# Kernel tuning notes

Measured on AMD Instinct MI355X. Metric: run time of the kernel, lower is better.

The kernel has to match this reference:

```python
import jax, jax.numpy as jnp
import numpy as np

RANK, A1, A2, B1, B2, BATCH = 16, 64, 8, 64, 8, 32768

def setup_inputs() -> dict:
    key = jax.random.key(0)
    kx, ks, ka, kb, kbias = jax.random.split(key, 5)
    # Params drawn as small gaussians (stand-in for xavier init; exact init
    x = jax.random.normal(kx, (BATCH, A1 * B1), dtype=jnp.float32)
    s = jax.random.normal(ks, (A1, A2), dtype=jnp.float32)
    a = jax.random.normal(ka, (RANK, A1, A2), dtype=jnp.float32) * 0.05
    b = jax.random.normal(kb, (RANK, B1, B2), dtype=jnp.float32) * 0.05
    bias = jax.random.normal(kbias, (A2 * B2,), dtype=jnp.float32)
    return {"x": x, "s": s, "a": a, "b": b, "bias": bias}

def reference(x, s, a, b, bias):
    # sa[r] = s * a[r]   (elementwise scale shared across ranks)
    sa = s[None, :, :] * a                                    # (r, a1, a2)
    # w = sum_r kron(sa[r], b[r]): w[i*b1+k, j*b2+l] = sum_r sa[r,i,j] b[r,k,l]
    # w is only (a1*b1, a2*b2) = (4096, 64), cheap to materialize here.
    w = jnp.einsum('rij,rkl->ikjl', sa, b).reshape(A1 * B1, A2 * B2)
    return x @ w + bias[None, :]                              # (batch, a2*b2)
```

## Files before the change

kernel.cpp:

```cpp
#include <hip/hip_runtime.h>
#include <hip/hip_bf16.h>

#define RANK 16
#define BATCH 32768
#define K_DIM 4096
#define N_DIM 64
#define CHUNK 128
#define NCHUNK 32
#define ROWB 64

typedef __bf16 bf16x8 __attribute__((ext_vector_type(8)));
typedef float floatx4 __attribute__((ext_vector_type(4)));
typedef unsigned short ushort8 __attribute__((ext_vector_type(8)));

__device__ inline unsigned short f2bf(float f) {
  unsigned u = __builtin_bit_cast(unsigned, f);
  u += 0x7fffu + ((u >> 16) & 1u);
  return (unsigned short)(u >> 16);
}

__device__ inline bf16x8 cvt8(float4 a0, float4 a1) {
  ushort8 au;
  au[0] = f2bf(a0.x); au[1] = f2bf(a0.y); au[2] = f2bf(a0.z); au[3] = f2bf(a0.w);
  au[4] = f2bf(a1.x); au[5] = f2bf(a1.y); au[6] = f2bf(a1.z); au[7] = f2bf(a1.w);
  return __builtin_bit_cast(bf16x8, au);
}

__global__ __launch_bounds__(256) void build_wT(
    const float* __restrict__ s, const float* __restrict__ a,
    const float* __restrict__ b, unsigned short* __restrict__ wT) {
  int idx = blockIdx.x * 256 + threadIdx.x;
  int n = idx >> 12;
  int k = idx & 4095;
  int j = n >> 3, l = n & 7;
  int i = k >> 6, kk = k & 63;
  float acc = 0.f;
  #pragma unroll
  for (int r = 0; r < RANK; ++r) {
    acc += a[r * 512 + i * 8 + j] * b[r * 512 + kk * 8 + l];
  }
  acc *= s[i * 8 + j];
  wT[idx] = f2bf(acc);
}

__global__ __launch_bounds__(256, 2) void kron_gemm(
    const float* __restrict__ x, const unsigned short* __restrict__ wT,
    const float* __restrict__ bias, float* __restrict__ out) {
  __shared__ __align__(16) float As[2][ROWB * CHUNK];

  const int tid   = threadIdx.x;
  const int lane  = tid & 63;
  const int wave  = tid >> 6;
  const int ln15  = lane & 15;
  const int kseg  = lane >> 4;
  const int u     = lane & 31;
  const int rhalf = lane >> 5;
  const int m0    = blockIdx.x * ROWB;
  const int sw    = (ln15 & 7) << 4;

  const unsigned short* wp = wT + (size_t)(wave * 16 + ln15) * K_DIM + kseg * 8;

  floatx4 acc[4] = {};

  auto stage = [&](int buf, int c) {
    #pragma unroll
    for (int j = 0; j < 8; ++j) {
      const int row = wave * 16 + 2 * j + rhalf;
      const int sb  = (u * 16) ^ ((row & 7) << 4);
      const float* src = x + (size_t)(m0 + row) * K_DIM + c * CHUNK + (sb >> 2);
      float* dst = &As[buf][(wave * 16 + 2 * j) * CHUNK];
      __builtin_amdgcn_global_load_lds(
          (const __attribute__((address_space(1))) void*)(const void*)src,
          (__attribute__((address_space(3))) void*)(void*)dst,
          16, 0, 0);
    }
  };

  stage(0, 0);
  __syncthreads();

  for (int c = 0; c < NCHUNK; ++c) {
    const int cur = c & 1;
    if (c + 1 < NCHUNK) stage(cur ^ 1, c + 1);

    const char* Ab = (const char*)&As[cur][0];
    #pragma unroll
    for (int t = 0; t < 4; ++t) {
      bf16x8 wf = *(const bf16x8*)(wp + c * CHUNK + t * 32);
      #pragma unroll
      for (int f = 0; f < 4; ++f) {
        const int row = 16 * f + ln15;
        const int b0  = t * 128 + kseg * 32;
        float4 lo = *(const float4*)(Ab + row * 512 + ((b0)      ^ sw));
        float4 hi = *(const float4*)(Ab + row * 512 + ((b0 + 16) ^ sw));
        acc[f] = __builtin_amdgcn_mfma_f32_16x16x32_bf16(cvt8(lo, hi), wf, acc[f], 0, 0, 0);
      }
    }
    __syncthreads();
  }

  const int col = wave * 16 + ln15;
  const float bv = bias[col];
  #pragma unroll
  for (int f = 0; f < 4; ++f) {
    float* op = out + (size_t)(m0 + 16 * f + kseg * 4) * N_DIM + col;
    #pragma unroll
    for (int r = 0; r < 4; ++r)
      op[(size_t)r * N_DIM] = acc[f][r] + bv;
  }
}

extern "C" void kernel_launch(void* const* d_in, const int* in_sizes, int n_in,
                              void* d_out, int out_size, void* d_ws, size_t ws_size,
                              hipStream_t stream) {
  const float* x    = (const float*)d_in[0];
  const float* s    = (const float*)d_in[1];
  const float* a    = (const float*)d_in[2];
  const float* b    = (const float*)d_in[3];
  const float* bias = (const float*)d_in[4];
  float* out = (float*)d_out;
  unsigned short* wT = (unsigned short*)d_ws;

  build_wT<<<(N_DIM * K_DIM) / 256, 256, 0, stream>>>(s, a, b, wT);
  kron_gemm<<<BATCH / ROWB, 256, 0, stream>>>(x, wT, bias, out);
}
```

Baseline: 138.3 us.

## Triple-buffer x and W tiles in LDS with 32x32 MFMA tiling

Each k-step now stages both the x tile and a fragment-ordered bf16 W tile into LDS through async global_load_lds into a three-deep ring. Waits use explicit vmcnt counts and raw barriers, replacing the previous double buffer, which read W straight from global memory per wave. The weight build kernel now writes W pre-permuted into the MFMA fragment layout. Compute switches from four 16x16x32 MFMAs per wave to one 32x32x16 MFMA per k-subtile on a 2x2 wave grid, with a smaller chunk of 64. Per-block LDS use rises and the hand-tuned vmcnt counts must exactly match the number of loads issued.

```diff
diff --git a/kernel.cpp b/kernel.cpp
--- a/kernel.cpp
+++ b/kernel.cpp
@@ -5,13 +5,17 @@
 #define BATCH 32768
 #define K_DIM 4096
 #define N_DIM 64
-#define CHUNK 128
-#define NCHUNK 32
+#define CHUNK 64
+#define NCHUNK 64
+#define NBUF 3
 #define ROWB 64
 
 typedef __bf16 bf16x8 __attribute__((ext_vector_type(8)));
-typedef float floatx4 __attribute__((ext_vector_type(4)));
+typedef float f32x16 __attribute__((ext_vector_type(16)));
 typedef unsigned short ushort8 __attribute__((ext_vector_type(8)));
+
+#define WAITVM(n) asm volatile("s_waitcnt vmcnt(" #n ")" ::: "memory")
+#define BARRIER() asm volatile("s_barrier" ::: "memory")
 
 __device__ inline unsigned short f2bf(float f) {
   unsigned u = __builtin_bit_cast(unsigned, f);
@@ -26,87 +30,105 @@
   return __builtin_bit_cast(bf16x8, au);
 }
 
-__global__ __launch_bounds__(256) void build_wT(
+__global__ __launch_bounds__(256) void build_wF(
     const float* __restrict__ s, const float* __restrict__ a,
-    const float* __restrict__ b, unsigned short* __restrict__ wT) {
-  int idx = blockIdx.x * 256 + threadIdx.x;
-  int n = idx >> 12;
-  int k = idx & 4095;
-  int j = n >> 3, l = n & 7;
-  int i = k >> 6, kk = k & 63;
+    const float* __restrict__ b, unsigned short* __restrict__ wF) {
+  int e = blockIdx.x * 256 + threadIdx.x;
+  int j  = e & 7;
+  int l  = (e >> 3) & 63;
+  int t  = (e >> 9) & 255;
+  int cb = e >> 17;
+  int n = cb * 32 + (l & 31);
+  int k = t * 16 + ((l >> 5) << 3) + j;
+  int i = k >> 6, kk = k & 63, jj = n >> 3, ll = n & 7;
   float acc = 0.f;
   #pragma unroll
   for (int r = 0; r < RANK; ++r) {
-    acc += a[r * 512 + i * 8 + j] * b[r * 512 + kk * 8 + l];
+    acc += a[r * 512 + i * 8 + jj] * b[r * 512 + kk * 8 + ll];
   }
-  acc *= s[i * 8 + j];
-  wT[idx] = f2bf(acc);
+  acc *= s[i * 8 + jj];
+  wF[e] = f2bf(acc);
 }
 
 __global__ __launch_bounds__(256, 2) void kron_gemm(
-    const float* __restrict__ x, const unsigned short* __restrict__ wT,
+    const float* __restrict__ x, const unsigned short* __restrict__ wF,
     const float* __restrict__ bias, float* __restrict__ out) {
-  __shared__ __align__(16) float As[2][ROWB * CHUNK];
+  __shared__ __align__(16) float  As[NBUF][ROWB * CHUNK];
+  __shared__ __align__(16) __bf16 Ws[NBUF][8][64 * 8];
 
-  const int tid   = threadIdx.x;
-  const int lane  = tid & 63;
-  const int wave  = tid >> 6;
-  const int ln15  = lane & 15;
-  const int kseg  = lane >> 4;
-  const int u     = lane & 31;
-  const int rhalf = lane >> 5;
-  const int m0    = blockIdx.x * ROWB;
-  const int sw    = (ln15 & 7) << 4;
+  const int tid  = threadIdx.x;
+  const int lane = tid & 63;
+  const int wave = tid >> 6;
+  const int qr   = wave & 1;
+  const int qc   = wave >> 1;
+  const int l31  = lane & 31;
+  const int hi   = lane >> 5;
+  const int m0   = blockIdx.x * ROWB;
+  const int arow = qr * 32 + l31;
+  const int aswz = (arow & 15) << 4;
 
-  const unsigned short* wp = wT + (size_t)(wave * 16 + ln15) * K_DIM + kseg * 8;
-
-  floatx4 acc[4] = {};
+  f32x16 acc;
+  #pragma unroll
+  for (int i = 0; i < 16; ++i) acc[i] = 0.f;
 
   auto stage = [&](int buf, int c) {
     #pragma unroll
-    for (int j = 0; j < 8; ++j) {
-      const int row = wave * 16 + 2 * j + rhalf;
-      const int sb  = (u * 16) ^ ((row & 7) << 4);
+    for (int p = 0; p < 4; ++p) {
+      const int rbase = wave * 16 + 4 * p;
+      const int row   = rbase + (lane >> 4);
+      const int sb    = (((lane & 15) ^ (row & 15)) << 4);
       const float* src = x + (size_t)(m0 + row) * K_DIM + c * CHUNK + (sb >> 2);
-      float* dst = &As[buf][(wave * 16 + 2 * j) * CHUNK];
+      float* dst = &As[buf][rbase * CHUNK];
       __builtin_amdgcn_global_load_lds(
           (const __attribute__((address_space(1))) void*)(const void*)src,
-          (__attribute__((address_space(3))) void*)(void*)dst,
-          16, 0, 0);
+          (__attribute__((address_space(3))) void*)(void*)dst, 16, 0, 0);
+    }
+    #pragma unroll
+    for (int p = 0; p < 2; ++p) {
+      const int idx = wave * 2 + p;
+      const int r = idx >> 2, sub = idx & 3;
+      const unsigned short* src =
+          wF + (((size_t)(r * 256 + c * 4 + sub)) << 9) + lane * 8;
+      __bf16* dst = &Ws[buf][r * 4 + sub][0];
+      __builtin_amdgcn_global_load_lds(
+          (const __attribute__((address_space(1))) void*)(const void*)src,
+          (__attribute__((address_space(3))) void*)(void*)dst, 16, 0, 0);
+    }
+  };
+
+  auto compute = [&](int buf) {
+    const char* Ab = (const char*)&As[buf][0];
+    #pragma unroll
+    for (int t = 0; t < 4; ++t) {
+      bf16x8 wf = *(const bf16x8*)&Ws[buf][qc * 4 + t][lane * 8];
+      const int colb = t * 64 + hi * 32;
+      float4 lo = *(const float4*)(Ab + arow * 256 + ((colb)      ^ aswz));
+      float4 h4 = *(const float4*)(Ab + arow * 256 + ((colb + 16) ^ aswz));
+      acc = __builtin_amdgcn_mfma_f32_32x32x16_bf16(cvt8(lo, h4), wf, acc, 0, 0, 0);
     }
   };
 
   stage(0, 0);
-  __syncthreads();
+  stage(1, 1);
 
-  for (int c = 0; c < NCHUNK; ++c) {
-    const int cur = c & 1;
-    if (c + 1 < NCHUNK) stage(cur ^ 1, c + 1);
+  int b0 = 0, b1 = 1, b2 = 2;
+  for (int c = 0; c < NCHUNK - 2; ++c) {
+    stage(b2, c + 2);
+    WAITVM(12);
+    BARRIER();
+    compute(b0);
+    BARRIER();
+    const int tmp = b0; b0 = b1; b1 = b2; b2 = tmp;
+  }
+  WAITVM(6);  BARRIER(); compute(b0);
+  WAITVM(0);  BARRIER(); compute(b1);
 
-    const char* Ab = (const char*)&As[cur][0];
-    #pragma unroll
-    for (int t = 0; t < 4; ++t) {
-      bf16x8 wf = *(const bf16x8*)(wp + c * CHUNK + t * 32);
-      #pragma unroll
-      for (int f = 0; f < 4; ++f) {
-        const int row = 16 * f + ln15;
-        const int b0  = t * 128 + kseg * 32;
-        float4 lo = *(const float4*)(Ab + row * 512 + ((b0)      ^ sw));
-        float4 hi = *(const float4*)(Ab + row * 512 + ((b0 + 16) ^ sw));
-        acc[f] = __builtin_amdgcn_mfma_f32_16x16x32_bf16(cvt8(lo, hi), wf, acc[f], 0, 0, 0);
-      }
-    }
-    __syncthreads();
-  }
-
-  const int col = wave * 16 + ln15;
+  const int col = qc * 32 + l31;
   const float bv = bias[col];
   #pragma unroll
-  for (int f = 0; f < 4; ++f) {
-    float* op = out + (size_t)(m0 + 16 * f + kseg * 4) * N_DIM + col;
-    #pragma unroll
-    for (int r = 0; r < 4; ++r)
-      op[(size_t)r * N_DIM] = acc[f][r] + bv;
+  for (int r = 0; r < 16; ++r) {
+    const int orow = (r & 3) + 8 * (r >> 2) + 4 * hi;
+    out[(size_t)(m0 + qr * 32 + orow) * N_DIM + col] = acc[r] + bv;
   }
 }
 
@@ -119,8 +141,8 @@
   const float* b    = (const float*)d_in[3];
   const float* bias = (const float*)d_in[4];
   float* out = (float*)d_out;
-  unsigned short* wT = (unsigned short*)d_ws;
+  unsigned short* wF = (unsigned short*)d_ws;
 
-  build_wT<<<(N_DIM * K_DIM) / 256, 256, 0, stream>>>(s, a, b, wT);
-  kron_gemm<<<BATCH / ROWB, 256, 0, stream>>>(x, wT, bias, out);
+  build_wF<<<1024, 256, 0, stream>>>(s, a, b, wF);
+  kron_gemm<<<BATCH / ROWB, 256, 0, stream>>>(x, wF, bias, out);
 }
```

After: 153.7 us. 1.11x slower.
